# Performance work log

Measured on AMD Instinct MI355X. Metric: run time of the kernel, lower is better.

## Reference

```python
import jax, jax.numpy as jnp
import numpy as np

NUM_RING = 16
MAX_RING = 1520
EPS = 1e-5


def setup_inputs() -> dict:
    key = jax.random.key(0)
    B, C, N = 16, 64, 16384
    cnt = N // NUM_RING  # 1024 points per ring, sorted
    k1, k2, k3, k4, k5 = jax.random.split(key, 5)
    x = jax.random.normal(k1, (B, C, N), dtype=jnp.float32)
    # ring ids: sorted, exactly cnt points per ring (the module assumes sorted,
    # identical-count rings across batch)
    ring = jnp.broadcast_to(jnp.arange(N, dtype=jnp.int64) // cnt, (B, N))
    # random-upsample indices: concat(arange(cnt), randperm(cnt)[:MAX_RING-cnt])
    rng = np.random.default_rng(0)
    up = MAX_RING - cnt  # 496
    choice = np.empty((B, NUM_RING, MAX_RING), dtype=np.int64)
    for b in range(B):
        for r in range(NUM_RING):
            choice[b, r, :cnt] = np.arange(cnt)
            choice[b, r, cnt:] = rng.permutation(cnt)[:up]
    choice = jnp.asarray(choice)
    # grouped Conv1d(64 -> 128, kernel 1, groups=16): weight [128, 4, 1] -> [16, 8, 4]
    Wg = jax.random.normal(k2, (NUM_RING, 8, 4), dtype=jnp.float32) * 0.5
    bias = jax.random.normal(k3, (128,), dtype=jnp.float32) * 0.1
    gamma = jnp.ones((128,), dtype=jnp.float32)
    beta = jnp.zeros((128,), dtype=jnp.float32)
    return {"x": x, "Wg": Wg, "bias": bias, "gamma": gamma, "beta": beta,
            "ring": ring, "choice": choice}


def reference(x, Wg, bias, gamma, beta, ring, choice):
    B, C, N = x.shape  # C = 64
    R, MR = NUM_RING, MAX_RING
    cnt = N // R
    L = R * MR  # 24320

    xt = jnp.transpose(x, (0, 2, 1))  # [B, N, 64]
    # per-ring gather with random upsample to MAX_RING points
    idx = (jnp.arange(R, dtype=choice.dtype)[None, :, None] * cnt + choice)  # [B,R,MR]
    gathered = jnp.take_along_axis(xt, idx.reshape(B, L, 1), axis=1)  # [B, L, 64]

    # faithful to torch: cat(...).view(B, 64, -1) is a raw reshape (channel-scrambling)
    xc = gathered.reshape(B, C, L)  # [B, 64, L]

    # grouped 1x1 conv: 16 groups, 4 in / 8 out channels each
    xg = xc.reshape(B, R, 4, L)
    y = jnp.einsum('goc,bgcl->bgol', Wg, xg).reshape(B, 128, L)
    y = y + bias[None, :, None]

    # BatchNorm1d (training mode: batch statistics, biased variance)
    mean = jnp.mean(y, axis=(0, 2))
    var = jnp.var(y, axis=(0, 2))
    y = gamma[None, :, None] * (y - mean[None, :, None]) * jax.lax.rsqrt(var + EPS)[None, :, None] + beta[None, :, None]

    # per-ring max over MAX_RING slots, broadcast back to original ring sizes
    pooled = jnp.max(y.reshape(B, 128, R, MR), axis=-1)  # [B, 128, R]
    out = jnp.repeat(pooled, cnt, axis=2)  # [B, 128, N]
    return out
```

## Files before the change

kernel.cpp:

```cpp
#include <hip/hip_runtime.h>
#include <float.h>

#define NB    16
#define CIN   64
#define NPT   16384
#define NRING 16
#define MAXR  1520
#define LTOT  (NRING*MAXR)
#define MBLK  380
#define NCH   128

typedef float fx4 __attribute__((ext_vector_type(4)));

__device__ __forceinline__ float sload(float v) {
    return __int_as_float(__builtin_amdgcn_readfirstlane(__float_as_int(v)));
}

template<int CTRL>
__device__ __forceinline__ float fdpp(float v) {
    return __int_as_float(__builtin_amdgcn_mov_dpp(__float_as_int(v), CTRL, 0xF, 0xF, true));
}
#define DPP_QP_XOR1 0xB1
#define DPP_QP_XOR2 0x4E
#define DPP_SHR1  0x111
#define DPP_SHR2  0x112
#define DPP_SHR4  0x114
#define DPP_SHR8  0x118
#define DPP_BC15  0x142
#define DPP_BC31  0x143

__device__ __forceinline__ void gl_lds16(const float* g, float* l) {
    __builtin_amdgcn_global_load_lds(
        (const __attribute__((address_space(1))) void*)g,
        (__attribute__((address_space(3))) void*)l, 16, 0, 0);
}

__global__ __launch_bounds__(256) void k1_gather_conv(
    const float* __restrict__ x, const float* __restrict__ Wg,
    const float* __restrict__ bias, const float* __restrict__ gamma,
    const int* __restrict__ choice,
    float* __restrict__ p_sum, float* __restrict__ p_sqs,
    float* __restrict__ p_max)
{
    __shared__ float xs[4][1024];
    __shared__ int   iw[4][384];

    const int blk = blockIdx.x;
    const int b  = blk >> 8;
    const int cp = (blk >> 2) & 63;
    const int q  = blk & 3;
    const int t  = threadIdx.x;
    const int w  = t >> 6;
    const int lane = t & 63;
    const int g  = q*4 + w;

    {
        const float* gb = x + ((size_t)(b*CIN + cp))*NPT + (g << 10) + lane*4;
        float* lb = &xs[w][0];
        gl_lds16(gb,       lb);
        gl_lds16(gb + 256, lb + 256);
        gl_lds16(gb + 512, lb + 512);
        gl_lds16(gb + 768, lb + 768);
    }

    {
        const int* __restrict__ cg = choice + ((size_t)(b*NRING + g))*MAXR;
        #pragma unroll
        for (int k = 0; k < 2; ++k) {
            const int j = lane + k*64;
            if (j < 95) {
                const int4 a = *(const int4*)(cg + 760  + 4*j);
                const int4 c = *(const int4*)(cg + 1140 + 4*j);
                int4 p;
                p.x = a.x | (c.x << 16); p.y = a.y | (c.y << 16);
                p.z = a.z | (c.z << 16); p.w = a.w | (c.w << 16);
                *(int4*)(&iw[w][4*j]) = p;
            }
        }
    }

    float wq[8][4], bq[8], sg8[8];
    #pragma unroll
    for (int o = 0; o < 8; ++o) {
        const int ch = g*8 + o;
        const float sgn = (gamma[ch] < 0.0f) ? -1.0f : 1.0f;
        sg8[o] = sload(sgn);
        bq[o]  = sload(sgn * bias[ch]);
        #pragma unroll
        for (int c = 0; c < 4; ++c) wq[o][c] = sload(sgn * Wg[ch*4 + c]);
    }

    const int r = lane >> 2;
    const int s = lane & 3;
    const int mlo = (r*MAXR - cp + 63) >> 6;
    int mhi = ((r+1)*MAXR - cp + 63) >> 6;
    if (mhi > MBLK) mhi = MBLK;
    const int m0 = mlo + s;

    asm volatile("s_waitcnt vmcnt(0)" ::: "memory");

    const float* __restrict__ xg  = &xs[w][0];
    const int*   __restrict__ igw = &iw[w][0];

    int wv[5];
    #pragma unroll
    for (int k = 0; k < 5; ++k) wv[k] = igw[m0 + 4*k];

    float smax[8], ssum[8], ssq[8];
    #pragma unroll
    for (int o = 0; o < 8; ++o) { smax[o] = -FLT_MAX; ssum[o] = 0.f; ssq[o] = 0.f; }

    #pragma unroll
    for (int k = 0; k < 5; ++k) {
        const int m  = m0 + 4*k;
        const int i2 = wv[k] & 0xFFFF;
        const int i3 = ((unsigned)wv[k]) >> 16;
        const float v0 = xg[m];
        const float v1 = xg[380 + m];
        const float v2 = xg[i2];
        const float v3 = xg[i3];
        #pragma unroll
        for (int o = 0; o < 8; ++o) {
            float y = fmaf(wq[o][0], v0, fmaf(wq[o][1], v1,
                      fmaf(wq[o][2], v2, fmaf(wq[o][3], v3, bq[o]))));
            smax[o] = fmaxf(smax[o], y);
            ssum[o] += y;
            ssq[o]  = fmaf(y, y, ssq[o]);
        }
    }
    {
        const int m = m0 + 20;
        if (m < mhi) {
            const int wt = igw[m];
            const int i2 = wt & 0xFFFF;
            const int i3 = ((unsigned)wt) >> 16;
            const float v0 = xg[m];
            const float v1 = xg[380 + m];
            const float v2 = xg[i2];
            const float v3 = xg[i3];
            #pragma unroll
            for (int o = 0; o < 8; ++o) {
                float y = fmaf(wq[o][0], v0, fmaf(wq[o][1], v1,
                          fmaf(wq[o][2], v2, fmaf(wq[o][3], v3, bq[o]))));
                smax[o] = fmaxf(smax[o], y);
                ssum[o] += y;
                ssq[o]  = fmaf(y, y, ssq[o]);
            }
        }
    }

    #pragma unroll
    for (int o = 0; o < 8; ++o) {
        smax[o] = fmaxf(smax[o], fdpp<DPP_QP_XOR1>(smax[o]));
        smax[o] = fmaxf(smax[o], fdpp<DPP_QP_XOR2>(smax[o]));
    }

    if (s == 0) {
        float* base = p_max + (((size_t)(b*64 + cp))*NRING + r)*NCH + g*8;
        ((float4*)base)[0] = make_float4(smax[0], smax[1], smax[2], smax[3]);
        ((float4*)base)[1] = make_float4(smax[4], smax[5], smax[6], smax[7]);
    }

    #pragma unroll
    for (int o = 0; o < 8; ++o) {
        ssum[o] += fdpp<DPP_SHR1>(ssum[o]);  ssq[o] += fdpp<DPP_SHR1>(ssq[o]);
        ssum[o] += fdpp<DPP_SHR2>(ssum[o]);  ssq[o] += fdpp<DPP_SHR2>(ssq[o]);
        ssum[o] += fdpp<DPP_SHR4>(ssum[o]);  ssq[o] += fdpp<DPP_SHR4>(ssq[o]);
        ssum[o] += fdpp<DPP_SHR8>(ssum[o]);  ssq[o] += fdpp<DPP_SHR8>(ssq[o]);
        ssum[o] += fdpp<DPP_BC15>(ssum[o]);  ssq[o] += fdpp<DPP_BC15>(ssq[o]);
        ssum[o] += fdpp<DPP_BC31>(ssum[o]);  ssq[o] += fdpp<DPP_BC31>(ssq[o]);
    }
    if (lane == 63) {
        float* baseS = p_sum + ((size_t)(b*64 + cp))*NCH + g*8;
        float* baseQ = p_sqs + ((size_t)(b*64 + cp))*NCH + g*8;
        ((float4*)baseS)[0] = make_float4(sg8[0]*ssum[0], sg8[1]*ssum[1], sg8[2]*ssum[2], sg8[3]*ssum[3]);
        ((float4*)baseS)[1] = make_float4(sg8[4]*ssum[4], sg8[5]*ssum[5], sg8[6]*ssum[6], sg8[7]*ssum[7]);
        ((float4*)baseQ)[0] = make_float4(ssq[0], ssq[1], ssq[2], ssq[3]);
        ((float4*)baseQ)[1] = make_float4(ssq[4], ssq[5], ssq[6], ssq[7]);
    }
}

__global__ __launch_bounds__(256) void k23_pool_bcast(
    const float* __restrict__ p_sum, const float* __restrict__ p_sqs,
    const float* __restrict__ p_max,
    const float* __restrict__ gamma, const float* __restrict__ beta,
    fx4* __restrict__ out)
{
    __shared__ float part[16][17];
    __shared__ float wsum[4], wsq[4];
    __shared__ float pool[16];
    const int bc = blockIdx.x;
    const int b  = bc >> 7;
    const int ch = bc & 127;
    const int t  = threadIdx.x;

    const int r = t >> 4, ck = t & 15;
    float v = -FLT_MAX;
    #pragma unroll
    for (int k = 0; k < 4; ++k) {
        const int cpi = ck*4 + k;
        v = fmaxf(v, p_max[(((size_t)(b*64 + cpi))*NRING + r)*NCH + ch]);
    }

    float S = 0.f, Q = 0.f;
    #pragma unroll
    for (int i = 0; i < 4; ++i) {
        const int jj = t + i*256;
        S += p_sum[(size_t)jj*NCH + ch];
        Q += p_sqs[(size_t)jj*NCH + ch];
    }
    #pragma unroll
    for (int off = 1; off < 64; off <<= 1) {
        S += __shfl_xor(S, off);
        Q += __shfl_xor(Q, off);
    }
    part[r][ck] = v;
    if ((t & 63) == 0) { wsum[t >> 6] = S; wsq[t >> 6] = Q; }
    __syncthreads();

    if (t < 16) {
        const float inv = 1.0f / (float)((size_t)NB * LTOT);
        const float Sa = wsum[0] + wsum[1] + wsum[2] + wsum[3];
        const float Qa = wsq[0] + wsq[1] + wsq[2] + wsq[3];
        const float mean = Sa * inv;
        const float var  = Qa * inv - mean*mean;
        const float istd = rsqrtf(var + 1e-5f);
        float acc = part[t][0];
        #pragma unroll
        for (int k = 1; k < 16; ++k) acc = fmaxf(acc, part[t][k]);
        const float gm = gamma[ch];
        const float raw = (gm >= 0.0f) ? acc : -acc;
        pool[t] = gm * (raw - mean) * istd + beta[ch];
    }
    __syncthreads();

    fx4* __restrict__ dst = out + (size_t)bc * (NPT/4);
    #pragma unroll
    for (int i = 0; i < 16; ++i) {
        const int idx = t + i*256;
        const float vv = pool[idx >> 8];
        fx4 val; val.x = vv; val.y = vv; val.z = vv; val.w = vv;
        __builtin_nontemporal_store(val, &dst[idx]);
    }
}

extern "C" void kernel_launch(void* const* d_in, const int* in_sizes, int n_in,
                              void* d_out, int out_size, void* d_ws, size_t ws_size,
                              hipStream_t stream)
{
    const float* x     = (const float*)d_in[0];
    const float* Wg    = (const float*)d_in[1];
    const float* bias  = (const float*)d_in[2];
    const float* gamma = (const float*)d_in[3];
    const float* beta  = (const float*)d_in[4];
    const int* choice  = (const int*)d_in[6];

    float* p_sum = (float*)d_ws;
    float* p_sqs = p_sum + (size_t)1024*NCH;
    float* p_max = p_sqs + (size_t)1024*NCH;

    k1_gather_conv<<<NB*CIN*4, 256, 0, stream>>>(x, Wg, bias, gamma, choice,
                                                 p_sum, p_sqs, p_max);
    k23_pool_bcast<<<NB*NCH, 256, 0, stream>>>(p_sum, p_sqs, p_max,
                                               gamma, beta, (fx4*)d_out);
}
```

Before: 62.30 us.

## Process four channel-planes per block with double-buffered LDS staging

Result: faster. 55.25 us (-11.3%).

```diff
diff --git a/kernel.cpp b/kernel.cpp
--- a/kernel.cpp
+++ b/kernel.cpp
@@ -42,98 +42,105 @@
     float* __restrict__ p_sum, float* __restrict__ p_sqs,
     float* __restrict__ p_max)
 {
-    __shared__ float xs[4][1024];
+    __shared__ float xs[2][4][1024];
     __shared__ int   iw[4][384];
 
     const int blk = blockIdx.x;
-    const int b  = blk >> 8;
-    const int cp = (blk >> 2) & 63;
-    const int q  = blk & 3;
-    const int t  = threadIdx.x;
-    const int w  = t >> 6;
+    const int cpg = blk & 15;
+    const int bq  = blk >> 4;
+    const int b   = bq >> 2;
+    const int q   = bq & 3;
+    const int cp0 = cpg << 2;
+    const int t    = threadIdx.x;
+    const int w    = t >> 6;
     const int lane = t & 63;
-    const int g  = q*4 + w;
-
-    {
-        const float* gb = x + ((size_t)(b*CIN + cp))*NPT + (g << 10) + lane*4;
-        float* lb = &xs[w][0];
-        gl_lds16(gb,       lb);
-        gl_lds16(gb + 256, lb + 256);
-        gl_lds16(gb + 512, lb + 512);
-        gl_lds16(gb + 768, lb + 768);
-    }
-
-    {
-        const int* __restrict__ cg = choice + ((size_t)(b*NRING + g))*MAXR;
-        #pragma unroll
-        for (int k = 0; k < 2; ++k) {
-            const int j = lane + k*64;
-            if (j < 95) {
-                const int4 a = *(const int4*)(cg + 760  + 4*j);
-                const int4 c = *(const int4*)(cg + 1140 + 4*j);
-                int4 p;
-                p.x = a.x | (c.x << 16); p.y = a.y | (c.y << 16);
-                p.z = a.z | (c.z << 16); p.w = a.w | (c.w << 16);
-                *(int4*)(&iw[w][4*j]) = p;
-            }
-        }
-    }
-
-    float wq[8][4], bq[8], sg8[8];
+    const int g    = q*4 + w;
+
+    const int* __restrict__ cg = choice + ((size_t)(b*NRING + g))*MAXR;
+    const int j1 = lane + 64;
+    int4 a0 = *(const int4*)(cg + 760  + 4*lane);
+    int4 c0 = *(const int4*)(cg + 1140 + 4*lane);
+    int4 a1 = make_int4(0,0,0,0), c1 = make_int4(0,0,0,0);
+    if (j1 < 95) {
+        a1 = *(const int4*)(cg + 760  + 4*j1);
+        c1 = *(const int4*)(cg + 1140 + 4*j1);
+    }
+    float gv[8], bv[8], w0[8], w1[8], w2[8], w3[8];
     #pragma unroll
     for (int o = 0; o < 8; ++o) {
         const int ch = g*8 + o;
-        const float sgn = (gamma[ch] < 0.0f) ? -1.0f : 1.0f;
+        gv[o] = gamma[ch]; bv[o] = bias[ch];
+        w0[o] = Wg[ch*4];  w1[o] = Wg[ch*4+1];
+        w2[o] = Wg[ch*4+2]; w3[o] = Wg[ch*4+3];
+    }
+    asm volatile("s_waitcnt vmcnt(0)" ::: "memory");
+
+    {
+        int4 p;
+        p.x = a0.x | (c0.x << 16); p.y = a0.y | (c0.y << 16);
+        p.z = a0.z | (c0.z << 16); p.w = a0.w | (c0.w << 16);
+        *(int4*)(&iw[w][4*lane]) = p;
+        if (j1 < 95) {
+            p.x = a1.x | (c1.x << 16); p.y = a1.y | (c1.y << 16);
+            p.z = a1.z | (c1.z << 16); p.w = a1.w | (c1.w << 16);
+            *(int4*)(&iw[w][4*j1]) = p;
+        }
+    }
+    float wq[8][4], bq8[8], sg8[8];
+    #pragma unroll
+    for (int o = 0; o < 8; ++o) {
+        const float sgn = (gv[o] < 0.0f) ? -1.0f : 1.0f;
         sg8[o] = sload(sgn);
-        bq[o]  = sload(sgn * bias[ch]);
-        #pragma unroll
-        for (int c = 0; c < 4; ++c) wq[o][c] = sload(sgn * Wg[ch*4 + c]);
-    }
+        bq8[o] = sload(sgn * bv[o]);
+        wq[o][0] = sload(sgn * w0[o]); wq[o][1] = sload(sgn * w1[o]);
+        wq[o][2] = sload(sgn * w2[o]); wq[o][3] = sload(sgn * w3[o]);
+    }
+
+    #define STAGE(bufi, cpv) do { \
+        const float* gb_ = x + ((size_t)(b*CIN + (cpv)))*NPT + (g << 10) + lane*4; \
+        float* lb_ = &xs[bufi][w][0]; \
+        gl_lds16(gb_,       lb_);       \
+        gl_lds16(gb_ + 256, lb_ + 256); \
+        gl_lds16(gb_ + 512, lb_ + 512); \
+        gl_lds16(gb_ + 768, lb_ + 768); \
+    } while (0)
+
+    STAGE(0, cp0);
+    STAGE(1, cp0 + 1);
 
     const int r = lane >> 2;
     const int s = lane & 3;
-    const int mlo = (r*MAXR - cp + 63) >> 6;
-    int mhi = ((r+1)*MAXR - cp + 63) >> 6;
-    if (mhi > MBLK) mhi = MBLK;
-    const int m0 = mlo + s;
-
-    asm volatile("s_waitcnt vmcnt(0)" ::: "memory");
-
-    const float* __restrict__ xg  = &xs[w][0];
-    const int*   __restrict__ igw = &iw[w][0];
-
-    int wv[5];
-    #pragma unroll
-    for (int k = 0; k < 5; ++k) wv[k] = igw[m0 + 4*k];
-
-    float smax[8], ssum[8], ssq[8];
-    #pragma unroll
-    for (int o = 0; o < 8; ++o) { smax[o] = -FLT_MAX; ssum[o] = 0.f; ssq[o] = 0.f; }
-
-    #pragma unroll
-    for (int k = 0; k < 5; ++k) {
-        const int m  = m0 + 4*k;
-        const int i2 = wv[k] & 0xFFFF;
-        const int i3 = ((unsigned)wv[k]) >> 16;
-        const float v0 = xg[m];
-        const float v1 = xg[380 + m];
-        const float v2 = xg[i2];
-        const float v3 = xg[i3];
-        #pragma unroll
-        for (int o = 0; o < 8; ++o) {
-            float y = fmaf(wq[o][0], v0, fmaf(wq[o][1], v1,
-                      fmaf(wq[o][2], v2, fmaf(wq[o][3], v3, bq[o]))));
-            smax[o] = fmaxf(smax[o], y);
-            ssum[o] += y;
-            ssq[o]  = fmaf(y, y, ssq[o]);
-        }
-    }
-    {
-        const int m = m0 + 20;
-        if (m < mhi) {
-            const int wt = igw[m];
-            const int i2 = wt & 0xFFFF;
-            const int i3 = ((unsigned)wt) >> 16;
+    const int* __restrict__ igw = &iw[w][0];
+
+    float smax[4][8], ssum[8], ssq[8];
+    #pragma unroll
+    for (int o = 0; o < 8; ++o) { ssum[o] = 0.f; ssq[o] = 0.f; }
+    #pragma unroll
+    for (int tt = 0; tt < 4; ++tt)
+        #pragma unroll
+        for (int o = 0; o < 8; ++o) smax[tt][o] = -FLT_MAX;
+
+    #pragma unroll
+    for (int tt = 0; tt < 4; ++tt) {
+        if (tt < 3) { asm volatile("s_waitcnt vmcnt(4)" ::: "memory"); }
+        else        { asm volatile("s_waitcnt vmcnt(0)" ::: "memory"); }
+
+        const int cp = cp0 + tt;
+        const float* __restrict__ xg = &xs[tt & 1][w][0];
+        const int mlo = (r*MAXR - cp + 63) >> 6;
+        int mhi = ((r+1)*MAXR - cp + 63) >> 6;
+        if (mhi > MBLK) mhi = MBLK;
+        const int m0 = mlo + s;
+
+        int wvk[5];
+        #pragma unroll
+        for (int k = 0; k < 5; ++k) wvk[k] = igw[m0 + 4*k];
+
+        #pragma unroll
+        for (int k = 0; k < 5; ++k) {
+            const int m  = m0 + 4*k;
+            const int i2 = wvk[k] & 0xFFFF;
+            const int i3 = ((unsigned)wvk[k]) >> 16;
             const float v0 = xg[m];
             const float v1 = xg[380 + m];
             const float v2 = xg[i2];
@@ -141,24 +148,49 @@
             #pragma unroll
             for (int o = 0; o < 8; ++o) {
                 float y = fmaf(wq[o][0], v0, fmaf(wq[o][1], v1,
-                          fmaf(wq[o][2], v2, fmaf(wq[o][3], v3, bq[o]))));
-                smax[o] = fmaxf(smax[o], y);
+                          fmaf(wq[o][2], v2, fmaf(wq[o][3], v3, bq8[o]))));
+                smax[tt][o] = fmaxf(smax[tt][o], y);
                 ssum[o] += y;
                 ssq[o]  = fmaf(y, y, ssq[o]);
             }
         }
-    }
-
-    #pragma unroll
-    for (int o = 0; o < 8; ++o) {
-        smax[o] = fmaxf(smax[o], fdpp<DPP_QP_XOR1>(smax[o]));
-        smax[o] = fmaxf(smax[o], fdpp<DPP_QP_XOR2>(smax[o]));
-    }
-
-    if (s == 0) {
-        float* base = p_max + (((size_t)(b*64 + cp))*NRING + r)*NCH + g*8;
-        ((float4*)base)[0] = make_float4(smax[0], smax[1], smax[2], smax[3]);
-        ((float4*)base)[1] = make_float4(smax[4], smax[5], smax[6], smax[7]);
+        {
+            const int m = m0 + 20;
+            if (m < mhi) {
+                const int wt = igw[m];
+                const int i2 = wt & 0xFFFF;
+                const int i3 = ((unsigned)wt) >> 16;
+                const float v0 = xg[m];
+                const float v1 = xg[380 + m];
+                const float v2 = xg[i2];
+                const float v3 = xg[i3];
+                #pragma unroll
+                for (int o = 0; o < 8; ++o) {
+                    float y = fmaf(wq[o][0], v0, fmaf(wq[o][1], v1,
+                              fmaf(wq[o][2], v2, fmaf(wq[o][3], v3, bq8[o]))));
+                    smax[tt][o] = fmaxf(smax[tt][o], y);
+                    ssum[o] += y;
+                    ssq[o]  = fmaf(y, y, ssq[o]);
+                }
+            }
+        }
+
+        if (tt < 2) STAGE(tt & 1, cp0 + tt + 2);
+    }
+    #undef STAGE
+
+    #pragma unroll
+    for (int tt = 0; tt < 4; ++tt) {
+        #pragma unroll
+        for (int o = 0; o < 8; ++o) {
+            smax[tt][o] = fmaxf(smax[tt][o], fdpp<DPP_QP_XOR1>(smax[tt][o]));
+            smax[tt][o] = fmaxf(smax[tt][o], fdpp<DPP_QP_XOR2>(smax[tt][o]));
+        }
+        if (s == 0) {
+            float* base = p_max + (((size_t)(b*64 + cp0 + tt))*NRING + r)*NCH + g*8;
+            ((float4*)base)[0] = make_float4(smax[tt][0], smax[tt][1], smax[tt][2], smax[tt][3]);
+            ((float4*)base)[1] = make_float4(smax[tt][4], smax[tt][5], smax[tt][6], smax[tt][7]);
+        }
     }
 
     #pragma unroll
@@ -171,8 +203,8 @@
         ssum[o] += fdpp<DPP_BC31>(ssum[o]);  ssq[o] += fdpp<DPP_BC31>(ssq[o]);
     }
     if (lane == 63) {
-        float* baseS = p_sum + ((size_t)(b*64 + cp))*NCH + g*8;
-        float* baseQ = p_sqs + ((size_t)(b*64 + cp))*NCH + g*8;
+        float* baseS = p_sum + (size_t)blk*32 + w*8;
+        float* baseQ = p_sqs + (size_t)blk*32 + w*8;
         ((float4*)baseS)[0] = make_float4(sg8[0]*ssum[0], sg8[1]*ssum[1], sg8[2]*ssum[2], sg8[3]*ssum[3]);
         ((float4*)baseS)[1] = make_float4(sg8[4]*ssum[4], sg8[5]*ssum[5], sg8[6]*ssum[6], sg8[7]*ssum[7]);
         ((float4*)baseQ)[0] = make_float4(ssq[0], ssq[1], ssq[2], ssq[3]);
@@ -193,6 +225,7 @@
     const int b  = bc >> 7;
     const int ch = bc & 127;
     const int t  = threadIdx.x;
+    const int q  = ch >> 5, c32 = ch & 31;
 
     const int r = t >> 4, ck = t & 15;
     float v = -FLT_MAX;
@@ -202,13 +235,10 @@
         v = fmaxf(v, p_max[(((size_t)(b*64 + cpi))*NRING + r)*NCH + ch]);
     }
 
-    float S = 0.f, Q = 0.f;
-    #pragma unroll
-    for (int i = 0; i < 4; ++i) {
-        const int jj = t + i*256;
-        S += p_sum[(size_t)jj*NCH + ch];
-        Q += p_sqs[(size_t)jj*NCH + ch];
-    }
+    const int b2 = t >> 4, cpg2 = t & 15;
+    const int kb = (((b2*4 + q) << 4) | cpg2);
+    float S = p_sum[(size_t)kb*32 + c32];
+    float Q = p_sqs[(size_t)kb*32 + c32];
     #pragma unroll
     for (int off = 1; off < 64; off <<= 1) {
         S += __shfl_xor(S, off);
@@ -256,11 +286,11 @@
     const int* choice  = (const int*)d_in[6];
 
     float* p_sum = (float*)d_ws;
-    float* p_sqs = p_sum + (size_t)1024*NCH;
-    float* p_max = p_sqs + (size_t)1024*NCH;
-
-    k1_gather_conv<<<NB*CIN*4, 256, 0, stream>>>(x, Wg, bias, gamma, choice,
-                                                 p_sum, p_sqs, p_max);
+    float* p_sqs = p_sum + (size_t)1024*32;
+    float* p_max = p_sqs + (size_t)1024*32;
+
+    k1_gather_conv<<<1024, 256, 0, stream>>>(x, Wg, bias, gamma, choice,
+                                             p_sum, p_sqs, p_max);
     k23_pool_bcast<<<NB*NCH, 256, 0, stream>>>(p_sum, p_sqs, p_max,
                                                gamma, beta, (fx4*)d_out);
 }
```
